# Optimization experiments

Measured on AMD Instinct MI355X. Metric: run time of the kernel, lower is better.

The kernel has to match this reference:

```python
import jax, jax.numpy as jnp
import numpy as np

DN = ('NHWC', 'HWIO', 'NHWC')
EPS = 1e-8
BN_EPS = 1e-3
ROUT_ITERS = 3


def _bn(x, p, axis):
    # p: [4, C] rows = gamma, beta, moving_mean, moving_var (inference-mode BN)
    shp = [1] * x.ndim
    shp[axis % x.ndim] = x.shape[axis % x.ndim]
    g, b, m, v = [p[i].reshape(shp) for i in range(4)]
    return (x - m) * jax.lax.rsqrt(v + BN_EPS) * g + b


def _conv(x, w, b, stride, pad):
    return jax.lax.conv_general_dilated(x, w, (stride, stride), pad, dimension_numbers=DN) + b


def _patches(x, k, s):
    # x: [B, H, W, ...] -> [B, Ho, Wo, k*k, ...] (static k*k strided slices, no big gathers)
    Ho = (x.shape[1] - k) // s + 1
    Wo = (x.shape[2] - k) // s + 1
    sl = [x[:, i:i + s * (Ho - 1) + 1:s, j:j + s * (Wo - 1) + 1:s]
          for i in range(k) for j in range(k)]
    return jnp.stack(sl, axis=3)


def _em_routing(votes, a_in, beta_a, beta_u, iters=ROUT_ITERS):
    # votes: [..., Nin, Nout, D], a_in: [..., Nin]; Hinton matrix-capsule EM routing
    Nout = votes.shape[-2]
    R = jnp.full(votes.shape[:-1], 1.0 / Nout, votes.dtype)  # [..., Nin, Nout]
    a_ex = a_in[..., None]
    for i in range(iters):
        lam = 0.01 * (i + 1)  # inverse-temperature schedule
        Ra = R * a_ex                                             # [..., Nin, Nout]
        Rs = Ra.sum(-2) + EPS                                     # [..., Nout]
        mu = jnp.einsum('...no,...nod->...od', Ra, votes) / Rs[..., None]
        diff2 = (votes - mu[..., None, :, :]) ** 2                # [..., Nin, Nout, D]
        sig2 = jnp.einsum('...no,...nod->...od', Ra, diff2) / Rs[..., None] + EPS
        cost = (beta_u[:, None] + 0.5 * jnp.log(sig2)) * Rs[..., None]
        a_out = jax.nn.sigmoid(lam * (beta_a - cost.sum(-1)))     # [..., Nout]
        if i < iters - 1:
            logp = -0.5 * jnp.sum(diff2 / sig2[..., None, :, :]
                                  + jnp.log(2.0 * jnp.pi * sig2)[..., None, :, :], axis=-1)
            R = jax.nn.softmax(jnp.log(a_out + EPS)[..., None, :] + logp, axis=-1)
    return mu, a_out


def _convcaps(pose, a, W, beta_a, beta_u, k=3, s=2):
    # pose: [B,H,W,C,4,4], a: [B,H,W,C]; W: [k*k*C, Cout, 4, 4]
    pp = _patches(pose, k, s)                  # [B,Ho,Wo,k*k,C,4,4]
    B, Ho, Wo = pp.shape[:3]
    pp = pp.reshape(B, Ho, Wo, -1, 4, 4)       # [B,Ho,Wo,Nin,4,4]
    ap = _patches(a, k, s).reshape(B, Ho, Wo, -1)
    Cout = W.shape[1]
    votes = jnp.einsum('bhwnij,nojk->bhwnoik', pp, W).reshape(B, Ho, Wo, pp.shape[3], Cout, 16)
    mu, a_out = _em_routing(votes, ap, beta_a, beta_u)
    return mu.reshape(B, Ho, Wo, Cout, 4, 4), a_out


def reference(x, conv_w, conv_b, bn1, prim_pose_w, prim_pose_b, prim_act_w, prim_act_b,
              bn2, cc1_w, cc1_ba, cc1_bu, bn3, cc2_w, cc2_ba, cc2_bu, bn4,
              dc_w, dc_ba, dc_bu, dec_w1, dec_b1, dec_w2, dec_b2, dec_w3, dec_b3):
    h = jax.nn.relu(_conv(x, conv_w, conv_b, 2, 'SAME'))          # conv1 + relu
    h = _bn(h, bn1, -1)
    pose = _conv(h, prim_pose_w, prim_pose_b, 2, 'VALID')         # PrimaryCaps pose conv
    B, H, W, _ = pose.shape
    pose = pose.reshape(B, H, W, 32, 4, 4)
    a = jax.nn.sigmoid(_conv(h, prim_act_w, prim_act_b, 2, 'VALID'))
    pose = _bn(pose, bn2, -3)
    pose, a = _convcaps(pose, a, cc1_w, cc1_ba, cc1_bu)
    pose = _bn(pose, bn3, -3)
    pose, a = _convcaps(pose, a, cc2_w, cc2_ba, cc2_bu)
    pose = _bn(pose, bn4, -3)
    # DenseCaps: flatten spatial grid of capsules
    pflat = pose.reshape(B, -1, 4, 4)                             # [B, 1152, 4, 4]
    aflat = a.reshape(B, -1)
    votes = jnp.einsum('bnij,nojk->bnoik', pflat, dc_w).reshape(B, pflat.shape[1], dc_w.shape[1], 16)
    mu, a_out = _em_routing(votes, aflat, dc_ba, dc_bu)           # mu: [B, 32, 16]
    dec_in = mu.reshape(B, -1)                                    # [B, 512]
    h = jax.nn.relu(dec_in @ dec_w1 + dec_b1)
    h = jax.nn.relu(h @ dec_w2 + dec_b2)
    return h @ dec_w3 + dec_b3


def _bn_params(k, C):
    k1, k2, k3, k4 = jax.random.split(k, 4)
    return jnp.stack([1.0 + 0.05 * jax.random.normal(k1, (C,)),
                      0.05 * jax.random.normal(k2, (C,)),
                      0.01 * jax.random.normal(k3, (C,)),
                      1.0 + 0.1 * jax.random.uniform(k4, (C,))]).astype(jnp.float32)


def setup_inputs() -> dict:
    key = jax.random.key(0)
    ks = jax.random.split(key, 24)
    B, HW, NV = 2, 128, 8192
    n = lambda k, s, sc: (sc * jax.random.normal(k, s)).astype(jnp.float32)
    return {
        'x': n(ks[0], (B, HW, HW, 3), 1.0),
        'conv_w': n(ks[1], (11, 11, 3, 96), 0.05), 'conv_b': n(ks[2], (96,), 0.05),
        'bn1': _bn_params(ks[3], 96),
        'prim_pose_w': n(ks[4], (9, 9, 96, 32 * 16), 0.05), 'prim_pose_b': n(ks[5], (32 * 16,), 0.05),
        'prim_act_w': n(ks[6], (9, 9, 96, 32), 0.05), 'prim_act_b': n(ks[7], (32,), 0.05),
        'bn2': _bn_params(ks[8], 32),
        'cc1_w': n(ks[9], (3 * 3 * 32, 32, 4, 4), 0.1),
        'cc1_ba': n(ks[10], (32,), 0.5), 'cc1_bu': n(ks[11], (32,), 0.5),
        'bn3': _bn_params(ks[12], 32),
        'cc2_w': n(ks[13], (3 * 3 * 32, 32, 4, 4), 0.1),
        'cc2_ba': n(ks[14], (32,), 0.5), 'cc2_bu': n(ks[15], (32,), 0.5),
        'bn4': _bn_params(ks[16], 32),
        'dc_w': n(ks[17], (6 * 6 * 32, 32, 4, 4), 0.1),
        'dc_ba': n(ks[18], (32,), 0.5), 'dc_bu': n(ks[19], (32,), 0.5),
        'dec_w1': n(ks[20], (512, 512), 0.05), 'dec_b1': jnp.zeros((512,), jnp.float32),
        'dec_w2': n(ks[21], (512, 1024), 0.05), 'dec_b2': jnp.zeros((1024,), jnp.float32),
        'dec_w3': n(ks[22], (1024, NV), 0.02), 'dec_b3': jnp.zeros((NV,), jnp.float32),
    }
```

## Files before the change

### kernel.cpp

```cpp
#include <hip/hip_runtime.h>
#include <hip/hip_bf16.h>

#define EPSR 1e-8f
#define BNEPS 1e-3f
#define LOG2PI 1.8378770664093453f

typedef _Float16 f16;
typedef _Float16 f16x4 __attribute__((ext_vector_type(4)));
typedef _Float16 f16x8 __attribute__((ext_vector_type(8)));
typedef float f32x4 __attribute__((ext_vector_type(4)));

#define O_H      0
#define O_POSE2  786432
#define O_ACT2   1589248
#define O_POSE3  1639424
#define O_ACT3   1812480
#define O_POSE4  1823296
#define O_ACT4   1860160
#define O_DECIN  1862464
#define O_H1     1863488
#define O_H2     1864512
#define O_PART   1866560
#define O_BWH    1997632
#define O_BWL    4485952
#define NEED_BYTES (6974272ull * 4ull)
#define O_DSTAT  0
#define O_DCOMB  32768

template<int F16>
__global__ __launch_bounds__(256) void conv1_k(
    const float* __restrict__ x, const float* __restrict__ w,
    const float* __restrict__ bias, const float* __restrict__ bn1,
    float* __restrict__ h32, f16* __restrict__ hh, f16* __restrict__ hl)
{
  int t = blockIdx.x * 256 + threadIdx.x;
  int c = t % 96; int px = t / 96;
  int ox = px & 63; int r = px >> 6; int oy = r & 63; int b = r >> 6;
  float acc = 0.f;
  int iy0 = 2*oy - 4, ix0 = 2*ox - 4;
  for (int ky = 0; ky < 11; ++ky) {
    int iy = iy0 + ky;
    if ((unsigned)iy > 127u) continue;
    const float* xrow = x + (size_t)((b*128 + iy)*128)*3;
    const float* wrow = w + (ky*11*3)*96 + c;
    for (int kx = 0; kx < 11; ++kx) {
      int ix = ix0 + kx;
      if ((unsigned)ix > 127u) continue;
      const float* xp = xrow + ix*3;
      const float* wp = wrow + kx*3*96;
      acc = fmaf(xp[0], wp[0],   acc);
      acc = fmaf(xp[1], wp[96],  acc);
      acc = fmaf(xp[2], wp[192], acc);
    }
  }
  acc += bias[c];
  acc = fmaxf(acc, 0.f);
  float g = bn1[c], be = bn1[96+c], mm = bn1[192+c], vv = bn1[288+c];
  float val = (acc - mm) * (g * rsqrtf(vv + BNEPS)) + be;
  if (F16) {
    f16 hi = (f16)val;
    f16 lo = (f16)(val - (float)hi);
    hh[t] = hi; hl[t] = lo;
  } else {
    h32[t] = val;
  }
}

__global__ __launch_bounds__(256) void split_w_k(
    const float* __restrict__ pw, const float* __restrict__ aw,
    f16* __restrict__ bwh, f16* __restrict__ bwl)
{
  __shared__ float tile[32][33];
  const int kb = blockIdx.x * 32, nb = blockIdx.y * 32;
  const int t = threadIdx.x;
  #pragma unroll
  for (int p = 0; p < 4; ++p) {
    int k_l = p*8 + (t>>5), n_l = t & 31;
    int k = kb + k_l, n = nb + n_l;
    float v = 0.f;
    if (n < 512) v = pw[(size_t)k*512 + n];
    else if (n < 544) v = aw[(size_t)k*32 + (n - 512)];
    tile[k_l][n_l] = v;
  }
  __syncthreads();
  #pragma unroll
  for (int p = 0; p < 4; ++p) {
    int n_l = p*8 + (t>>5), k_l = t & 31;
    float v = tile[k_l][n_l];
    f16 hi = (f16)v;
    f16 lo = (f16)(v - (float)hi);
    size_t dst = (size_t)(nb + n_l)*7776 + kb + k_l;
    bwh[dst] = hi; bwl[dst] = lo;
  }
}

__global__ __launch_bounds__(256) void zero_raw(float* __restrict__ pose2, float* __restrict__ act2)
{
  int t = blockIdx.x * 256 + threadIdx.x;
  if (t < 802816) pose2[t] = 0.f;
  else act2[t - 802816] = 0.f;
}

__global__ __launch_bounds__(256, 2) void conv2_mfma(
    const f16* __restrict__ hh, const f16* __restrict__ hl,
    const f16* __restrict__ bwh, const f16* __restrict__ bwl,
    float* __restrict__ pose2r, float* __restrict__ act2r)
{
  __shared__ f16 Ah[128*32];
  __shared__ f16 Al[128*32];
  __shared__ f16 Bh[128*32];
  __shared__ f16 Bl[128*32];
  const int tid = threadIdx.x;
  const int mb = blockIdx.x, nb = blockIdx.y, z = blockIdx.z;
  const int m0 = mb*128, n0 = nb*128;
  const int q = 243 / 8, rch = 243 % 8;
  const int k0 = z*q + (z < rch ? z : rch);
  const int k1 = k0 + q + (z < rch ? 1 : 0);

  const int srow = tid >> 3;
  const int c    = tid & 7;
  int habase[4]; bool amok[4];
  #pragma unroll
  for (int p = 0; p < 4; ++p) {
    int m = m0 + p*32 + srow;
    amok[p] = m < 1568;
    int mm = amok[p] ? m : 0;
    int b = mm / 784; int yx = mm - b*784; int oy = yx / 28, ox = yx - oy*28;
    habase[p] = ((b*64 + 2*oy)*64 + 2*ox)*96;
  }
  size_t bbase[4];
  #pragma unroll
  for (int p = 0; p < 4; ++p) bbase[p] = (size_t)(n0 + p*32 + srow) * 7776;

  f16x4 rah[4], ral[4], rbh[4], rbl[4];
  const f16x4 zv = {(f16)0, (f16)0, (f16)0, (f16)0};

  auto load_step = [&](int kt) {
    int ky = kt / 27, rr = kt % 27; int kx = rr / 3, ci0 = (rr % 3) * 32;
    int aoff = (ky*64 + kx)*96 + ci0 + c*4;
    int koff = kt*32 + c*4;
    #pragma unroll
    for (int p = 0; p < 4; ++p) {
      if (amok[p]) {
        rah[p] = *(const f16x4*)(hh + habase[p] + aoff);
        ral[p] = *(const f16x4*)(hl + habase[p] + aoff);
      } else { rah[p] = zv; ral[p] = zv; }
      rbh[p] = *(const f16x4*)(bwh + bbase[p] + koff);
      rbl[p] = *(const f16x4*)(bwl + bbase[p] + koff);
    }
  };

  int widx[4];
  #pragma unroll
  for (int p = 0; p < 4; ++p) {
    int row = p*32 + srow;
    widx[p] = row*32 + ((((c>>1) + (row>>1)) & 3) << 3) + ((c & 1) << 2);
  }

  const int wv = tid >> 6, lane = tid & 63;
  const int wr = wv >> 1, wc = wv & 1;
  const int l15 = lane & 15, g = lane >> 4;

  f32x4 acc[4][4];
  #pragma unroll
  for (int i = 0; i < 4; ++i)
    #pragma unroll
    for (int j = 0; j < 4; ++j) acc[i][j] = (f32x4){0.f, 0.f, 0.f, 0.f};

  int aidx[4], bidx[4];
  #pragma unroll
  for (int i = 0; i < 4; ++i) {
    int arow = wr*64 + i*16 + l15;
    aidx[i] = arow*32 + (((g + (arow>>1)) & 3) << 3);
    int brow = wc*64 + i*16 + l15;
    bidx[i] = brow*32 + (((g + (brow>>1)) & 3) << 3);
  }

  load_step(k0);
  for (int kt = k0; kt < k1; ++kt) {
    __syncthreads();
    #pragma unroll
    for (int p = 0; p < 4; ++p) {
      *(f16x4*)&Ah[widx[p]] = rah[p];
      *(f16x4*)&Al[widx[p]] = ral[p];
      *(f16x4*)&Bh[widx[p]] = rbh[p];
      *(f16x4*)&Bl[widx[p]] = rbl[p];
    }
    __syncthreads();
    if (kt + 1 < k1) load_step(kt + 1);
    f16x8 ah[4], al[4], bh[4], bl[4];
    #pragma unroll
    for (int i = 0; i < 4; ++i) {
      ah[i] = *(const f16x8*)&Ah[aidx[i]];
      al[i] = *(const f16x8*)&Al[aidx[i]];
      bh[i] = *(const f16x8*)&Bh[bidx[i]];
      bl[i] = *(const f16x8*)&Bl[bidx[i]];
    }
    #pragma unroll
    for (int i = 0; i < 4; ++i)
      #pragma unroll
      for (int j = 0; j < 4; ++j) {
        acc[i][j] = __builtin_amdgcn_mfma_f32_16x16x32_f16(ah[i], bh[j], acc[i][j], 0, 0, 0);
        acc[i][j] = __builtin_amdgcn_mfma_f32_16x16x32_f16(ah[i], bl[j], acc[i][j], 0, 0, 0);
        acc[i][j] = __builtin_amdgcn_mfma_f32_16x16x32_f16(al[i], bh[j], acc[i][j], 0, 0, 0);
      }
  }

  #pragma unroll
  for (int i = 0; i < 4; ++i) {
    #pragma unroll
    for (int j = 0; j < 4; ++j) {
      #pragma unroll
      for (int r2 = 0; r2 < 4; ++r2) {
        int m = m0 + wr*64 + i*16 + g*4 + r2;
        int n = n0 + wc*64 + j*16 + l15;
        if (m < 1568) {
          float val = acc[i][j][r2];
          if (n < 512) atomicAdd(&pose2r[(size_t)m*512 + n], val);
          else if (n < 544) atomicAdd(&act2r[(size_t)m*32 + (n - 512)], val);
        }
      }
    }
  }
}

__global__ __launch_bounds__(256) void conv2_gemm_ks(
    const float* __restrict__ h,
    const float* __restrict__ pw, const float* __restrict__ aw,
    float* __restrict__ pose2r, float* __restrict__ act2r)
{
  __shared__ float As[2][16][68];
  __shared__ float Bs[2][16][68];
  const int tid = threadIdx.x;
  const int mb = blockIdx.x, nb = blockIdx.y, z = blockIdx.z;
  const int m0 = mb * 64;
  const float* Bp; int ldB, n0;
  if (nb < 8) { Bp = pw; ldB = 512; n0 = nb * 64; } else { Bp = aw; ldB = 32; n0 = 0; }

  const int a_ml = tid & 63, a_cig = tid >> 6;
  const int am = m0 + a_ml;
  const bool am_ok = am < 1568;
  int ab_ = am / 784; int ayx = am - ab_*784;
  int aoy = ayx / 28, aox = ayx - aoy*28;
  if (!am_ok) { ab_ = 0; aoy = 0; aox = 0; }
  const float* a_base = h + (size_t)((ab_*64 + 2*aoy)*64 + 2*aox)*96 + a_cig*4;

  const int b_kk = tid >> 4, b_ng = tid & 15;
  const int b_col = b_ng * 4;
  const bool b_ok = b_col < ldB;

  const int tm = (tid & 15) * 4, tn = (tid >> 4) * 4;
  float acc[4][4] = {{0}};

  auto kidx = [](int kt, int& ky, int& kx, int& ci0) {
    int cig = kt % 6; int r = kt / 6; kx = r % 9; ky = r / 9; ci0 = cig * 16;
  };
  auto ldAv = [&](int ky, int kx, int ci0) -> float4 {
    if (!am_ok) return make_float4(0,0,0,0);
    return *(const float4*)(a_base + (ky*64 + kx)*96 + ci0);
  };
  auto ldBv = [&](int kt) -> float4 {
    if (!b_ok) return make_float4(0,0,0,0);
    return *(const float4*)(Bp + (size_t)(kt*16 + b_kk) * ldB + n0 + b_col);
  };
  auto wrAv = [&](float4 v, int buf) {
    As[buf][a_cig*4+0][a_ml] = v.x;
    As[buf][a_cig*4+1][a_ml] = v.y;
    As[buf][a_cig*4+2][a_ml] = v.z;
    As[buf][a_cig*4+3][a_ml] = v.w;
  };
  auto wrBv = [&](float4 v, int buf) {
    *(float4*)&Bs[buf][b_kk][b_col] = v;
  };

  const int kt0 = z * 81;
  {
    int ky, kx, ci0; kidx(kt0, ky, kx, ci0);
    wrAv(ldAv(ky, kx, ci0), 0); wrBv(ldBv(kt0), 0);
  }
  __syncthreads();

  for (int i = 0; i < 81; ++i) {
    int cur = i & 1;
    bool st = i < 80;
    float4 va, vb;
    if (st) {
      int ky, kx, ci0; kidx(kt0 + i + 1, ky, kx, ci0);
      va = ldAv(ky, kx, ci0);
      vb = ldBv(kt0 + i + 1);
    }
    #pragma unroll
    for (int kk = 0; kk < 16; ++kk) {
      float4 av = *(const float4*)&As[cur][kk][tm];
      float4 bv = *(const float4*)&Bs[cur][kk][tn];
      float aa[4] = {av.x, av.y, av.z, av.w};
      float bb4[4] = {bv.x, bv.y, bv.z, bv.w};
      #pragma unroll
      for (int ii = 0; ii < 4; ++ii)
        #pragma unroll
        for (int jj = 0; jj < 4; ++jj)
          acc[ii][jj] = fmaf(aa[ii], bb4[jj], acc[ii][jj]);
    }
    if (st) { wrAv(va, cur ^ 1); wrBv(vb, cur ^ 1); }
    __syncthreads();
  }

  #pragma unroll
  for (int i = 0; i < 4; ++i) {
    int m = m0 + tm + i;
    if (m >= 1568) break;
    #pragma unroll
    for (int j = 0; j < 4; ++j) {
      int nl = tn + j;
      if (nb < 8) {
        atomicAdd(&pose2r[(size_t)m*512 + n0 + nl], acc[i][j]);
      } else if (nl < 32) {
        atomicAdd(&act2r[(size_t)m*32 + nl], acc[i][j]);
      }
    }
  }
}

__global__ __launch_bounds__(256) void conv2_epi(
    const float* __restrict__ pb, const float* __restrict__ ab,
    const float* __restrict__ bn2,
    float* __restrict__ pose2, float* __restrict__ act2)
{
  int t = blockIdx.x * 256 + threadIdx.x;
  if (t < 802816) {
    int n = t & 511;
    float val = pose2[t] + pb[n];
    int caps = n >> 4;
    float g = bn2[caps], be = bn2[32+caps], mm = bn2[64+caps], vv = bn2[96+caps];
    pose2[t] = (val - mm) * (g * rsqrtf(vv + BNEPS)) + be;
  } else {
    int t2 = t - 802816;
    int nl = t2 & 31;
    float val = act2[t2] + ab[nl];
    act2[t2] = 1.f / (1.f + expf(-val));
  }
}

template<int NIN, int NWAVES, bool CONV>
__global__ __launch_bounds__(NWAVES*64) void routing_k(
    const float* __restrict__ pose_in, const float* __restrict__ act_in,
    const float* __restrict__ Wv,
    const float* __restrict__ ba, const float* __restrict__ bu,
    const float* __restrict__ bn,
    float* __restrict__ pose_out, float* __restrict__ act_out,
    int Hin, int Win, int Wout)
{
  constexpr int NT  = NWAVES * 64;
  constexpr int NPW = NIN / NWAVES;
  __shared__ float s1s[NWAVES][32*17];
  __shared__ float s2s[NWAVES][32*17];
  __shared__ float rsP[NWAVES][32];
  __shared__ float muS[32*17], isgS[32*17], lgS[32*17];
  __shared__ float laS[32], lsS[32], aoS[32], RsS[32], S0S[32];

  const int tid = threadIdx.x;
  const int wv = tid >> 6, lane = tid & 63;
  const int o = lane & 31, half = lane >> 5;

  int bb = 0, oy = 0, ox = 0;
  if (CONV) {
    int px = blockIdx.x;
    ox = px % Wout; int t2 = px / Wout; oy = t2 % Wout; bb = t2 / Wout;
  } else {
    bb = blockIdx.x;
  }

  float mur[8], isgr[8], lar = 0.f, lsr = 0.f;
  #pragma unroll
  for (int i = 0; i < 8; ++i) { mur[i] = 0.f; isgr[i] = 0.f; }

  for (int p = 0; p < 3; ++p) {
    float lam = 0.01f * (float)(p + 1);
    float s1r[8] = {0,0,0,0,0,0,0,0};
    float s2r[8] = {0,0,0,0,0,0,0,0};
    float rsr = 0.f;

    for (int it = 0; it < NPW; ++it) {
      int n = wv * NPW + it;
      const float* wp = Wv + (size_t)(n*32 + o) * 16;
      float4 w0 = *(const float4*)(wp);
      float4 w1 = *(const float4*)(wp + 4);
      float4 w2 = *(const float4*)(wp + 8);
      float4 w3 = *(const float4*)(wp + 12);
      const float* pp; float an;
      if (CONV) {
        int cc = n & 31, kk = n >> 5;
        int ki = kk / 3, kj = kk - ki*3;
        int pix = (bb*Hin + 2*oy + ki)*Win + 2*ox + kj;
        pp = pose_in + (size_t)(pix*32 + cc) * 16;
        an = act_in[pix*32 + cc];
      } else {
        pp = pose_in + (size_t)(bb*NIN + n) * 16;
        an = act_in[bb*NIN + n];
      }
      float4 p0 = *(const float4*)(pp + half*8);
      float4 p1 = *(const float4*)(pp + half*8 + 4);
      float v[8];
      v[0] = fmaf(p0.x,w0.x, fmaf(p0.y,w1.x, fmaf(p0.z,w2.x, p0.w*w3.x)));
      v[1] = fmaf(p0.x,w0.y, fmaf(p0.y,w1.y, fmaf(p0.z,w2.y, p0.w*w3.y)));
      v[2] = fmaf(p0.x,w0.z, fmaf(p0.y,w1.z, fmaf(p0.z,w2.z, p0.w*w3.z)));
      v[3] = fmaf(p0.x,w0.w, fmaf(p0.y,w1.w, fmaf(p0.z,w2.w, p0.w*w3.w)));
      v[4] = fmaf(p1.x,w0.x, fmaf(p1.y,w1.x, fmaf(p1.z,w2.x, p1.w*w3.x)));
      v[5] = fmaf(p1.x,w0.y, fmaf(p1.y,w1.y, fmaf(p1.z,w2.y, p1.w*w3.y)));
      v[6] = fmaf(p1.x,w0.z, fmaf(p1.y,w1.z, fmaf(p1.z,w2.z, p1.w*w3.z)));
      v[7] = fmaf(p1.x,w0.w, fmaf(p1.y,w1.w, fmaf(p1.z,w2.w, p1.w*w3.w)));

      float R;
      if (p == 0) {
        R = 1.f / 32.f;
      } else {
        float t = 0.f;
        #pragma unroll
        for (int dd = 0; dd < 8; ++dd) { float df = v[dd] - mur[dd]; t = fmaf(df*df, isgr[dd], t); }
        t += __shfl_xor(t, 32, 64);
        float logit = lar - 0.5f * (t + lsr);
        float mx = logit;
        mx = fmaxf(mx, __shfl_xor(mx, 16, 64));
        mx = fmaxf(mx, __shfl_xor(mx,  8, 64));
        mx = fmaxf(mx, __shfl_xor(mx,  4, 64));
        mx = fmaxf(mx, __shfl_xor(mx,  2, 64));
        mx = fmaxf(mx, __shfl_xor(mx,  1, 64));
        float e = expf(logit - mx);
        float se = e;
        se += __shfl_xor(se, 16, 64);
        se += __shfl_xor(se,  8, 64);
        se += __shfl_xor(se,  4, 64);
        se += __shfl_xor(se,  2, 64);
        se += __shfl_xor(se,  1, 64);
        R = e / se;
      }
      float Ra = R * an;
      rsr += Ra;
      #pragma unroll
      for (int dd = 0; dd < 8; ++dd) {
        s1r[dd] = fmaf(Ra, v[dd], s1r[dd]);
        s2r[dd] = fmaf(Ra * v[dd], v[dd], s2r[dd]);
      }
    }

    #pragma unroll
    for (int dd = 0; dd < 8; ++dd) {
      s1s[wv][o*17 + half*8 + dd] = s1r[dd];
      s2s[wv][o*17 + half*8 + dd] = s2r[dd];
    }
    if (!half) rsP[wv][o] = rsr;
    __syncthreads();
    if (tid < 32) {
      float r = 0.f;
      #pragma unroll
      for (int w2 = 0; w2 < NWAVES; ++w2) r += rsP[w2][tid];
      S0S[tid] = r; RsS[tid] = r + EPSR;
    }
    __syncthreads();
    for (int idx = tid; idx < 512; idx += NT) {
      int oo = idx >> 4, d = idx & 15;
      float S1 = 0.f, S2 = 0.f;
      #pragma unroll
      for (int w2 = 0; w2 < NWAVES; ++w2) { S1 += s1s[w2][oo*17+d]; S2 += s2s[w2][oo*17+d]; }
      float Rs = RsS[oo];
      float m_ = S1 / Rs;
      float sg = (S2 - 2.f*m_*S1 + m_*m_*S0S[oo]) / Rs + EPSR;
      muS[oo*17+d]  = m_;
      isgS[oo*17+d] = 1.f / sg;
      lgS[oo*17+d]  = logf(sg);
    }
    __syncthreads();
    if (tid < 32) {
      float L = 0.f;
      #pragma unroll
      for (int d = 0; d < 16; ++d) L += lgS[tid*17 + d];
      float cost = (16.f*bu[tid] + 0.5f*L) * RsS[tid];
      float av = 1.f / (1.f + expf(-lam * (ba[tid] - cost)));
      aoS[tid] = av;
      laS[tid] = logf(av + EPSR);
      lsS[tid] = 16.f*LOG2PI + L;
    }
    __syncthreads();
    if (p < 2) {
      #pragma unroll
      for (int dd = 0; dd < 8; ++dd) {
        mur[dd]  = muS[o*17 + half*8 + dd];
        isgr[dd] = isgS[o*17 + half*8 + dd];
      }
      lar = laS[o]; lsr = lsS[o];
    }
  }

  if (CONV) {
    int pxo = (bb*Wout + oy)*Wout + ox;
    for (int idx = tid; idx < 512; idx += NT) {
      int oo = idx >> 4, d = idx & 15;
      float val = muS[oo*17 + d];
      float g = bn[oo], be = bn[32+oo], mm = bn[64+oo], vv = bn[96+oo];
      val = (val - mm) * (g * rsqrtf(vv + BNEPS)) + be;
      pose_out[(size_t)pxo*512 + idx] = val;
    }
    if (tid < 32) act_out[(size_t)pxo*32 + tid] = aoS[tid];
  } else {
    for (int idx = tid; idx < 512; idx += NT)
      pose_out[(size_t)bb*512 + idx] = muS[(idx>>4)*17 + (idx&15)];
  }
}

template<int P>
__global__ __launch_bounds__(256) void dense_stats(
    const float* __restrict__ pose_in, const float* __restrict__ act_in,
    const float* __restrict__ Wv, const float* __restrict__ comb,
    float* __restrict__ stat)
{
  __shared__ float s1s[4][32*17];
  __shared__ float s2s[4][32*17];
  __shared__ float rsP[4][32];
  const int tid = threadIdx.x;
  const int wv = tid >> 6, lane = tid & 63;
  const int o = lane & 31, half = lane >> 5;
  const int bb = blockIdx.x / 12, chunk = blockIdx.x % 12;

  float mur[8], isgr[8], lar = 0.f, lsr = 0.f;
  if (P > 0) {
    const float* cb = comb + (size_t)bb * 1088;
    #pragma unroll
    for (int dd = 0; dd < 8; ++dd) {
      mur[dd]  = cb[o*16 + half*8 + dd];
      isgr[dd] = cb[512 + o*16 + half*8 + dd];
    }
    lar = cb[1024 + o]; lsr = cb[1056 + o];
  }

  float s1r[8] = {0,0,0,0,0,0,0,0};
  float s2r[8] = {0,0,0,0,0,0,0,0};
  float rsr = 0.f;

  for (int it = 0; it < 24; ++it) {
    int n = chunk*96 + wv*24 + it;
    const float* wp = Wv + (size_t)(n*32 + o) * 16;
    float4 w0 = *(const float4*)(wp);
    float4 w1 = *(const float4*)(wp + 4);
    float4 w2 = *(const float4*)(wp + 8);
    float4 w3 = *(const float4*)(wp + 12);
    const float* pp = pose_in + (size_t)(bb*1152 + n) * 16;
    float an = act_in[bb*1152 + n];
    float4 p0 = *(const float4*)(pp + half*8);
    float4 p1 = *(const float4*)(pp + half*8 + 4);
    float v[8];
    v[0] = fmaf(p0.x,w0.x, fmaf(p0.y,w1.x, fmaf(p0.z,w2.x, p0.w*w3.x)));
    v[1] = fmaf(p0.x,w0.y, fmaf(p0.y,w1.y, fmaf(p0.z,w2.y, p0.w*w3.y)));
    v[2] = fmaf(p0.x,w0.z, fmaf(p0.y,w1.z, fmaf(p0.z,w2.z, p0.w*w3.z)));
    v[3] = fmaf(p0.x,w0.w, fmaf(p0.y,w1.w, fmaf(p0.z,w2.w, p0.w*w3.w)));
    v[4] = fmaf(p1.x,w0.x, fmaf(p1.y,w1.x, fmaf(p1.z,w2.x, p1.w*w3.x)));
    v[5] = fmaf(p1.x,w0.y, fmaf(p1.y,w1.y, fmaf(p1.z,w2.y, p1.w*w3.y)));
    v[6] = fmaf(p1.x,w0.z, fmaf(p1.y,w1.z, fmaf(p1.z,w2.z, p1.w*w3.z)));
    v[7] = fmaf(p1.x,w0.w, fmaf(p1.y,w1.w, fmaf(p1.z,w2.w, p1.w*w3.w)));

    float R;
    if (P == 0) {
      R = 1.f / 32.f;
    } else {
      float t = 0.f;
      #pragma unroll
      for (int dd = 0; dd < 8; ++dd) { float df = v[dd] - mur[dd]; t = fmaf(df*df, isgr[dd], t); }
      t += __shfl_xor(t, 32, 64);
      float logit = lar - 0.5f * (t + lsr);
      float mx = logit;
      mx = fmaxf(mx, __shfl_xor(mx, 16, 64));
      mx = fmaxf(mx, __shfl_xor(mx,  8, 64));
      mx = fmaxf(mx, __shfl_xor(mx,  4, 64));
      mx = fmaxf(mx, __shfl_xor(mx,  2, 64));
      mx = fmaxf(mx, __shfl_xor(mx,  1, 64));
      float e = expf(logit - mx);
      float se = e;
      se += __shfl_xor(se, 16, 64);
      se += __shfl_xor(se,  8, 64);
      se += __shfl_xor(se,  4, 64);
      se += __shfl_xor(se,  2, 64);
      se += __shfl_xor(se,  1, 64);
      R = e / se;
    }
    float Ra = R * an;
    rsr += Ra;
    #pragma unroll
    for (int dd = 0; dd < 8; ++dd) {
      s1r[dd] = fmaf(Ra, v[dd], s1r[dd]);
      s2r[dd] = fmaf(Ra * v[dd], v[dd], s2r[dd]);
    }
  }

  #pragma unroll
  for (int dd = 0; dd < 8; ++dd) {
    s1s[wv][o*17 + half*8 + dd] = s1r[dd];
    s2s[wv][o*17 + half*8 + dd] = s2r[dd];
  }
  if (!half) rsP[wv][o] = rsr;
  __syncthreads();

  float* out = stat + (size_t)(bb*12 + chunk) * 1056;
  for (int idx = tid; idx < 512; idx += 256) {
    int oo = idx >> 4, d = idx & 15;
    float S1 = 0.f, S2 = 0.f;
    #pragma unroll
    for (int w2 = 0; w2 < 4; ++w2) { S1 += s1s[w2][oo*17+d]; S2 += s2s[w2][oo*17+d]; }
    out[idx] = S1; out[512 + idx] = S2;
  }
  if (tid < 32) {
    float r = 0.f;
    #pragma unroll
    for (int w2 = 0; w2 < 4; ++w2) r += rsP[w2][tid];
    out[1024 + tid] = r;
  }
}

template<int P>
__global__ __launch_bounds__(256) void dense_comb(
    const float* __restrict__ stat,
    const float* __restrict__ ba, const float* __restrict__ bu,
    float* __restrict__ comb, float* __restrict__ decin)
{
  __shared__ float S0S[32], RsS[32], lgS[32*17];
  const int tid = threadIdx.x;
  const int bb = blockIdx.x;
  const float* st = stat + (size_t)bb * 12 * 1056;
  float* cb = comb + (size_t)bb * 1088;

  if (tid < 32) {
    float r = 0.f;
    #pragma unroll
    for (int c = 0; c < 12; ++c) r += st[c*1056 + 1024 + tid];
    S0S[tid] = r; RsS[tid] = r + EPSR;
  }
  __syncthreads();
  for (int idx = tid; idx < 512; idx += 256) {
    int oo = idx >> 4, d = idx & 15;
    float S1 = 0.f, S2 = 0.f;
    #pragma unroll
    for (int c = 0; c < 12; ++c) { S1 += st[c*1056 + idx]; S2 += st[c*1056 + 512 + idx]; }
    float Rs = RsS[oo];
    float m_ = S1 / Rs;
    float sg = (S2 - 2.f*m_*S1 + m_*m_*S0S[oo]) / Rs + EPSR;
    if (P == 2) {
      decin[(size_t)bb*512 + idx] = m_;
    } else {
      cb[idx] = m_;
      cb[512 + idx] = 1.f / sg;
    }
    lgS[oo*17 + d] = logf(sg);
  }
  __syncthreads();
  if (P < 2 && tid < 32) {
    float L = 0.f;
    #pragma unroll
    for (int d = 0; d < 16; ++d) L += lgS[tid*17 + d];
    float lam = 0.01f * (float)(P + 1);
    float cost = (16.f*bu[tid] + 0.5f*L) * RsS[tid];
    float av = 1.f / (1.f + expf(-lam * (ba[tid] - cost)));
    cb[1024 + tid] = logf(av + EPSR);
    cb[1056 + tid] = 16.f*LOG2PI + L;
  }
}

__global__ __launch_bounds__(256) void fc_partial(
    const float* __restrict__ in, const float* __restrict__ W,
    float* __restrict__ part, int K, int N, int CK)
{
  int t = blockIdx.x * 256 + threadIdx.x;
  int nj = N >> 2;
  int j4 = t % nj, ks = t / nj;
  int k0 = ks * CK;
  float4 a0 = make_float4(0,0,0,0), a1 = make_float4(0,0,0,0);
  const float4* Wp = (const float4*)W;
  for (int kk = 0; kk < CK; ++kk) {
    int k = k0 + kk;
    float4 wv = Wp[(size_t)k * nj + j4];
    float f0 = in[k], f1 = in[K + k];
    a0.x = fmaf(f0, wv.x, a0.x); a0.y = fmaf(f0, wv.y, a0.y);
    a0.z = fmaf(f0, wv.z, a0.z); a0.w = fmaf(f0, wv.w, a0.w);
    a1.x = fmaf(f1, wv.x, a1.x); a1.y = fmaf(f1, wv.y, a1.y);
    a1.z = fmaf(f1, wv.z, a1.z); a1.w = fmaf(f1, wv.w, a1.w);
  }
  ((float4*)part)[(size_t)(ks*2 + 0) * nj + j4] = a0;
  ((float4*)part)[(size_t)(ks*2 + 1) * nj + j4] = a1;
}

__global__ __launch_bounds__(256) void fc_reduce(
    const float* __restrict__ part, const float* __restrict__ bias,
    float* __restrict__ out, int N, int KS, int relu)
{
  int t = blockIdx.x * 256 + threadIdx.x;
  int b = t / N, j = t - b*N;
  float s = bias[j];
  for (int ks = 0; ks < KS; ++ks) s += part[(size_t)(ks*2 + b) * N + j];
  if (relu) s = fmaxf(s, 0.f);
  out[(size_t)b*N + j] = s;
}

extern "C" void kernel_launch(void* const* d_in, const int* in_sizes, int n_in,
                              void* d_out, int out_size, void* d_ws, size_t ws_size,
                              hipStream_t stream) {
  const float* x    = (const float*)d_in[0];
  const float* c1w  = (const float*)d_in[1];
  const float* c1b  = (const float*)d_in[2];
  const float* bn1  = (const float*)d_in[3];
  const float* ppw  = (const float*)d_in[4];
  const float* ppb  = (const float*)d_in[5];
  const float* paw  = (const float*)d_in[6];
  const float* pab  = (const float*)d_in[7];
  const float* bn2  = (const float*)d_in[8];
  const float* ccw1 = (const float*)d_in[9];
  const float* cba1 = (const float*)d_in[10];
  const float* cbu1 = (const float*)d_in[11];
  const float* bn3  = (const float*)d_in[12];
  const float* ccw2 = (const float*)d_in[13];
  const float* cba2 = (const float*)d_in[14];
  const float* cbu2 = (const float*)d_in[15];
  const float* bn4  = (const float*)d_in[16];
  const float* dcw  = (const float*)d_in[17];
  const float* dcba = (const float*)d_in[18];
  const float* dcbu = (const float*)d_in[19];
  const float* w1   = (const float*)d_in[20];
  const float* b1   = (const float*)d_in[21];
  const float* w2   = (const float*)d_in[22];
  const float* b2   = (const float*)d_in[23];
  const float* w3   = (const float*)d_in[24];
  const float* b3   = (const float*)d_in[25];

  float* ws    = (float*)d_ws;
  float* h     = ws + O_H;
  f16*   hh    = (f16*)(ws + O_H);
  f16*   hl    = hh + 786432;
  float* pose2 = ws + O_POSE2;
  float* act2  = ws + O_ACT2;
  float* pose3 = ws + O_POSE3;
  float* act3  = ws + O_ACT3;
  float* pose4 = ws + O_POSE4;
  float* act4  = ws + O_ACT4;
  float* decin = ws + O_DECIN;
  float* h1    = ws + O_H1;
  float* h2    = ws + O_H2;
  float* part  = ws + O_PART;
  f16*   bwh   = (f16*)(ws + O_BWH);
  f16*   bwl   = (f16*)(ws + O_BWL);
  float* dstat = ws + O_DSTAT;
  float* dcomb = ws + O_DCOMB;

  const bool fast = ws_size >= NEED_BYTES;

  if (fast) {
    conv1_k<1><<<3072, 256, 0, stream>>>(x, c1w, c1b, bn1, nullptr, hh, hl);
    split_w_k<<<dim3(243, 20), 256, 0, stream>>>(ppw, paw, bwh, bwl);
    zero_raw<<<3332, 256, 0, stream>>>(pose2, act2);
    conv2_mfma<<<dim3(13, 5, 8), 256, 0, stream>>>(hh, hl, bwh, bwl, pose2, act2);
  } else {
    conv1_k<0><<<3072, 256, 0, stream>>>(x, c1w, c1b, bn1, h, nullptr, nullptr);
    zero_raw<<<3332, 256, 0, stream>>>(pose2, act2);
    conv2_gemm_ks<<<dim3(25, 9, 6), 256, 0, stream>>>(h, ppw, paw, pose2, act2);
  }
  conv2_epi<<<3332, 256, 0, stream>>>(ppb, pab, bn2, pose2, act2);
  routing_k<288, 8, true><<<338, 512, 0, stream>>>(pose2, act2, ccw1, cba1, cbu1, bn3,
                                                   pose3, act3, 28, 28, 13);
  routing_k<288, 8, true><<<72, 512, 0, stream>>>(pose3, act3, ccw2, cba2, cbu2, bn4,
                                                  pose4, act4, 13, 13, 6);
  dense_stats<0><<<24, 256, 0, stream>>>(pose4, act4, dcw, nullptr, dstat);
  dense_comb<0><<<2, 256, 0, stream>>>(dstat, dcba, dcbu, dcomb, nullptr);
  dense_stats<1><<<24, 256, 0, stream>>>(pose4, act4, dcw, dcomb, dstat);
  dense_comb<1><<<2, 256, 0, stream>>>(dstat, dcba, dcbu, dcomb, nullptr);
  dense_stats<2><<<24, 256, 0, stream>>>(pose4, act4, dcw, dcomb, dstat);
  dense_comb<2><<<2, 256, 0, stream>>>(dstat, dcba, dcbu, dcomb, decin);
  fc_partial<<<8, 256, 0, stream>>>(decin, w1, part, 512, 512, 32);
  fc_reduce<<<4, 256, 0, stream>>>(part, b1, h1, 512, 16, 1);
  fc_partial<<<16, 256, 0, stream>>>(h1, w2, part, 512, 1024, 32);
  fc_reduce<<<8, 256, 0, stream>>>(part, b2, h2, 1024, 16, 1);
  fc_partial<<<64, 256, 0, stream>>>(h2, w3, part, 1024, 8192, 128);
  fc_reduce<<<64, 256, 0, stream>>>(part, b3, (float*)d_out, 8192, 8, 0);
}
```

Baseline: 696.7 us.

## Prefetch next routing inputs, double routing block waves, finer FC split-K

The routing and dense-stats loops now load the next input capsule's weights, pose and activation before computing on the current one, so global-load latency overlaps with the vote and softmax math. The convolutional routing kernels run with 16 waves per 1024-thread block instead of 8 waves per 512-thread block. The decoder FC layers use more blocks with smaller K chunks, giving more parallel partial sums. The prefetch raises register pressure, and the larger blocks may reduce occupancy, add more shared-memory partials and lengthen the barrier reductions.

```diff
diff --git a/kernel.cpp b/kernel.cpp
--- a/kernel.cpp
+++ b/kernel.cpp
@@ -370,6 +370,28 @@
     bb = blockIdx.x;
   }
 
+  auto ld_n = [&](int n, float4& W0, float4& W1, float4& W2, float4& W3,
+                  float4& P0, float4& P1, float& AN) {
+    const float* wp = Wv + (size_t)(n*32 + o) * 16;
+    W0 = *(const float4*)(wp);
+    W1 = *(const float4*)(wp + 4);
+    W2 = *(const float4*)(wp + 8);
+    W3 = *(const float4*)(wp + 12);
+    const float* pp;
+    if (CONV) {
+      int cc = n & 31, kk = n >> 5;
+      int ki = kk / 3, kj = kk - ki*3;
+      int pix = (bb*Hin + 2*oy + ki)*Win + 2*ox + kj;
+      pp = pose_in + (size_t)(pix*32 + cc) * 16;
+      AN = act_in[pix*32 + cc];
+    } else {
+      pp = pose_in + (size_t)(bb*NIN + n) * 16;
+      AN = act_in[bb*NIN + n];
+    }
+    P0 = *(const float4*)(pp + half*8);
+    P1 = *(const float4*)(pp + half*8 + 4);
+  };
+
   float mur[8], isgr[8], lar = 0.f, lsr = 0.f;
   #pragma unroll
   for (int i = 0; i < 8; ++i) { mur[i] = 0.f; isgr[i] = 0.f; }
@@ -380,35 +402,22 @@
     float s2r[8] = {0,0,0,0,0,0,0,0};
     float rsr = 0.f;
 
+    float4 w0, w1, w2, w3, p0, p1; float an;
+    ld_n(wv*NPW, w0, w1, w2, w3, p0, p1, an);
+
     for (int it = 0; it < NPW; ++it) {
-      int n = wv * NPW + it;
-      const float* wp = Wv + (size_t)(n*32 + o) * 16;
-      float4 w0 = *(const float4*)(wp);
-      float4 w1 = *(const float4*)(wp + 4);
-      float4 w2 = *(const float4*)(wp + 8);
-      float4 w3 = *(const float4*)(wp + 12);
-      const float* pp; float an;
-      if (CONV) {
-        int cc = n & 31, kk = n >> 5;
-        int ki = kk / 3, kj = kk - ki*3;
-        int pix = (bb*Hin + 2*oy + ki)*Win + 2*ox + kj;
-        pp = pose_in + (size_t)(pix*32 + cc) * 16;
-        an = act_in[pix*32 + cc];
-      } else {
-        pp = pose_in + (size_t)(bb*NIN + n) * 16;
-        an = act_in[bb*NIN + n];
-      }
-      float4 p0 = *(const float4*)(pp + half*8);
-      float4 p1 = *(const float4*)(pp + half*8 + 4);
+      float4 cw0=w0, cw1=w1, cw2=w2, cw3=w3, cp0=p0, cp1=p1; float can=an;
+      if (it + 1 < NPW) ld_n(wv*NPW + it + 1, w0, w1, w2, w3, p0, p1, an);
+
       float v[8];
-      v[0] = fmaf(p0.x,w0.x, fmaf(p0.y,w1.x, fmaf(p0.z,w2.x, p0.w*w3.x)));
-      v[1] = fmaf(p0.x,w0.y, fmaf(p0.y,w1.y, fmaf(p0.z,w2.y, p0.w*w3.y)));
-      v[2] = fmaf(p0.x,w0.z, fmaf(p0.y,w1.z, fmaf(p0.z,w2.z, p0.w*w3.z)));
-      v[3] = fmaf(p0.x,w0.w, fmaf(p0.y,w1.w, fmaf(p0.z,w2.w, p0.w*w3.w)));
-      v[4] = fmaf(p1.x,w0.x, fmaf(p1.y,w1.x, fmaf(p1.z,w2.x, p1.w*w3.x)));
-      v[5] = fmaf(p1.x,w0.y, fmaf(p1.y,w1.y, fmaf(p1.z,w2.y, p1.w*w3.y)));
-      v[6] = fmaf(p1.x,w0.z, fmaf(p1.y,w1.z, fmaf(p1.z,w2.z, p1.w*w3.z)));
-      v[7] = fmaf(p1.x,w0.w, fmaf(p1.y,w1.w, fmaf(p1.z,w2.w, p1.w*w3.w)));
+      v[0] = fmaf(cp0.x,cw0.x, fmaf(cp0.y,cw1.x, fmaf(cp0.z,cw2.x, cp0.w*cw3.x)));
+      v[1] = fmaf(cp0.x,cw0.y, fmaf(cp0.y,cw1.y, fmaf(cp0.z,cw2.y, cp0.w*cw3.y)));
+      v[2] = fmaf(cp0.x,cw0.z, fmaf(cp0.y,cw1.z, fmaf(cp0.z,cw2.z, cp0.w*cw3.z)));
+      v[3] = fmaf(cp0.x,cw0.w, fmaf(cp0.y,cw1.w, fmaf(cp0.z,cw2.w, cp0.w*cw3.w)));
+      v[4] = fmaf(cp1.x,cw0.x, fmaf(cp1.y,cw1.x, fmaf(cp1.z,cw2.x, cp1.w*cw3.x)));
+      v[5] = fmaf(cp1.x,cw0.y, fmaf(cp1.y,cw1.y, fmaf(cp1.z,cw2.y, cp1.w*cw3.y)));
+      v[6] = fmaf(cp1.x,cw0.z, fmaf(cp1.y,cw1.z, fmaf(cp1.z,cw2.z, cp1.w*cw3.z)));
+      v[7] = fmaf(cp1.x,cw0.w, fmaf(cp1.y,cw1.w, fmaf(cp1.z,cw2.w, cp1.w*cw3.w)));
 
       float R;
       if (p == 0) {
@@ -434,7 +443,7 @@
         se += __shfl_xor(se,  1, 64);
         R = e / se;
       }
-      float Ra = R * an;
+      float Ra = R * can;
       rsr += Ra;
       #pragma unroll
       for (int dd = 0; dd < 8; ++dd) {
@@ -532,30 +541,39 @@
     lar = cb[1024 + o]; lsr = cb[1056 + o];
   }
 
+  auto ld_n = [&](int n, float4& W0, float4& W1, float4& W2, float4& W3,
+                  float4& P0, float4& P1, float& AN) {
+    const float* wp = Wv + (size_t)(n*32 + o) * 16;
+    W0 = *(const float4*)(wp);
+    W1 = *(const float4*)(wp + 4);
+    W2 = *(const float4*)(wp + 8);
+    W3 = *(const float4*)(wp + 12);
+    const float* pp = pose_in + (size_t)(bb*1152 + n) * 16;
+    AN = act_in[bb*1152 + n];
+    P0 = *(const float4*)(pp + half*8);
+    P1 = *(const float4*)(pp + half*8 + 4);
+  };
+
   float s1r[8] = {0,0,0,0,0,0,0,0};
   float s2r[8] = {0,0,0,0,0,0,0,0};
   float rsr = 0.f;
 
+  float4 w0, w1, w2, w3, p0, p1; float an;
+  ld_n(chunk*96 + wv*24, w0, w1, w2, w3, p0, p1, an);
+
   for (int it = 0; it < 24; ++it) {
-    int n = chunk*96 + wv*24 + it;
-    const float* wp = Wv + (size_t)(n*32 + o) * 16;
-    float4 w0 = *(const float4*)(wp);
-    float4 w1 = *(const float4*)(wp + 4);
-    float4 w2 = *(const float4*)(wp + 8);
-    float4 w3 = *(const float4*)(wp + 12);
-    const float* pp = pose_in + (size_t)(bb*1152 + n) * 16;
-    float an = act_in[bb*1152 + n];
-    float4 p0 = *(const float4*)(pp + half*8);
-    float4 p1 = *(const float4*)(pp + half*8 + 4);
+    float4 cw0=w0, cw1=w1, cw2=w2, cw3=w3, cp0=p0, cp1=p1; float can=an;
+    if (it + 1 < 24) ld_n(chunk*96 + wv*24 + it + 1, w0, w1, w2, w3, p0, p1, an);
+
     float v[8];
-    v[0] = fmaf(p0.x,w0.x, fmaf(p0.y,w1.x, fmaf(p0.z,w2.x, p0.w*w3.x)));
-    v[1] = fmaf(p0.x,w0.y, fmaf(p0.y,w1.y, fmaf(p0.z,w2.y, p0.w*w3.y)));
-    v[2] = fmaf(p0.x,w0.z, fmaf(p0.y,w1.z, fmaf(p0.z,w2.z, p0.w*w3.z)));
-    v[3] = fmaf(p0.x,w0.w, fmaf(p0.y,w1.w, fmaf(p0.z,w2.w, p0.w*w3.w)));
-    v[4] = fmaf(p1.x,w0.x, fmaf(p1.y,w1.x, fmaf(p1.z,w2.x, p1.w*w3.x)));
-    v[5] = fmaf(p1.x,w0.y, fmaf(p1.y,w1.y, fmaf(p1.z,w2.y, p1.w*w3.y)));
-    v[6] = fmaf(p1.x,w0.z, fmaf(p1.y,w1.z, fmaf(p1.z,w2.z, p1.w*w3.z)));
-    v[7] = fmaf(p1.x,w0.w, fmaf(p1.y,w1.w, fmaf(p1.z,w2.w, p1.w*w3.w)));
+    v[0] = fmaf(cp0.x,cw0.x, fmaf(cp0.y,cw1.x, fmaf(cp0.z,cw2.x, cp0.w*cw3.x)));
+    v[1] = fmaf(cp0.x,cw0.y, fmaf(cp0.y,cw1.y, fmaf(cp0.z,cw2.y, cp0.w*cw3.y)));
+    v[2] = fmaf(cp0.x,cw0.z, fmaf(cp0.y,cw1.z, fmaf(cp0.z,cw2.z, cp0.w*cw3.z)));
+    v[3] = fmaf(cp0.x,cw0.w, fmaf(cp0.y,cw1.w, fmaf(cp0.z,cw2.w, cp0.w*cw3.w)));
+    v[4] = fmaf(cp1.x,cw0.x, fmaf(cp1.y,cw1.x, fmaf(cp1.z,cw2.x, cp1.w*cw3.x)));
+    v[5] = fmaf(cp1.x,cw0.y, fmaf(cp1.y,cw1.y, fmaf(cp1.z,cw2.y, cp1.w*cw3.y)));
+    v[6] = fmaf(cp1.x,cw0.z, fmaf(cp1.y,cw1.z, fmaf(cp1.z,cw2.z, cp1.w*cw3.z)));
+    v[7] = fmaf(cp1.x,cw0.w, fmaf(cp1.y,cw1.w, fmaf(cp1.z,cw2.w, cp1.w*cw3.w)));
 
     float R;
     if (P == 0) {
@@ -581,7 +599,7 @@
       se += __shfl_xor(se,  1, 64);
       R = e / se;
     }
-    float Ra = R * an;
+    float Ra = R * can;
     rsr += Ra;
     #pragma unroll
     for (int dd = 0; dd < 8; ++dd) {
@@ -759,20 +777,20 @@
     conv2_gemm_ks<<<dim3(25, 9, 6), 256, 0, stream>>>(h, ppw, paw, pose2, act2);
   }
   conv2_epi<<<3332, 256, 0, stream>>>(ppb, pab, bn2, pose2, act2);
-  routing_k<288, 8, true><<<338, 512, 0, stream>>>(pose2, act2, ccw1, cba1, cbu1, bn3,
-                                                   pose3, act3, 28, 28, 13);
-  routing_k<288, 8, true><<<72, 512, 0, stream>>>(pose3, act3, ccw2, cba2, cbu2, bn4,
-                                                  pose4, act4, 13, 13, 6);
+  routing_k<288, 16, true><<<338, 1024, 0, stream>>>(pose2, act2, ccw1, cba1, cbu1, bn3,
+                                                     pose3, act3, 28, 28, 13);
+  routing_k<288, 16, true><<<72, 1024, 0, stream>>>(pose3, act3, ccw2, cba2, cbu2, bn4,
+                                                    pose4, act4, 13, 13, 6);
   dense_stats<0><<<24, 256, 0, stream>>>(pose4, act4, dcw, nullptr, dstat);
   dense_comb<0><<<2, 256, 0, stream>>>(dstat, dcba, dcbu, dcomb, nullptr);
   dense_stats<1><<<24, 256, 0, stream>>>(pose4, act4, dcw, dcomb, dstat);
   dense_comb<1><<<2, 256, 0, stream>>>(dstat, dcba, dcbu, dcomb, nullptr);
   dense_stats<2><<<24, 256, 0, stream>>>(pose4, act4, dcw, dcomb, dstat);
   dense_comb<2><<<2, 256, 0, stream>>>(dstat, dcba, dcbu, dcomb, decin);
-  fc_partial<<<8, 256, 0, stream>>>(decin, w1, part, 512, 512, 32);
-  fc_reduce<<<4, 256, 0, stream>>>(part, b1, h1, 512, 16, 1);
-  fc_partial<<<16, 256, 0, stream>>>(h1, w2, part, 512, 1024, 32);
-  fc_reduce<<<8, 256, 0, stream>>>(part, b2, h2, 1024, 16, 1);
-  fc_partial<<<64, 256, 0, stream>>>(h2, w3, part, 1024, 8192, 128);
-  fc_reduce<<<64, 256, 0, stream>>>(part, b3, (float*)d_out, 8192, 8, 0);
-}
+  fc_partial<<<16, 256, 0, stream>>>(decin, w1, part, 512, 512, 16);
+  fc_reduce<<<4, 256, 0, stream>>>(part, b1, h1, 512, 32, 1);
+  fc_partial<<<32, 256, 0, stream>>>(h1, w2, part, 512, 1024, 16);
+  fc_reduce<<<8, 256, 0, stream>>>(part, b2, h2, 1024, 32, 1);
+  fc_partial<<<256, 256, 0, stream>>>(h2, w3, part, 1024, 8192, 32);
+  fc_reduce<<<64, 256, 0, stream>>>(part, b3, (float*)d_out, 8192, 32, 0);
+}
```

Result: faster. 679.5 us (-2.5%).
